# Kernel optimization log

Hardware: AMD Instinct MI355X
Metric: run time of the kernel (lower is better)

## Reference

```python
import jax, jax.numpy as jnp
import numpy as np

D, U, NNZ, B = 8192, 4096, 1_700_000, 1024

def setup_inputs() -> dict:
    key = jax.random.key(0)
    k1, k2, k3, k4 = jax.random.split(key, 4)
    x = jax.random.normal(k1, (B, D), dtype=jnp.float32)
    kernel_vector = jax.random.normal(k2, (NNZ,), dtype=jnp.float32) * 0.02
    bias = jax.random.normal(k3, (U,), dtype=jnp.float32) * 0.01
    flat = jax.random.randint(k4, (NNZ,), 0, D * U)  # random sparsity pattern
    nonzero_ind = jnp.stack([flat // U, flat % U], axis=1).astype(jnp.int32)  # [NNZ, 2]
    return {"x": x, "kernel_vector": kernel_vector, "bias": bias, "nonzero_ind": nonzero_ind}

def reference(x, kernel_vector, bias, nonzero_ind):
    # scatter_nd: build dense (D, U) kernel from nonzero entries (duplicates add, as in tf.scatter_nd)
    W = jnp.zeros((D, U), dtype=kernel_vector.dtype).at[nonzero_ind[:, 0], nonzero_ind[:, 1]].add(kernel_vector)
    out = x @ W + bias  # [B, U]
    return jnp.tanh(out)
```

## Files before the change

### kernel.cpp

```cpp
#include <hip/hip_runtime.h>
#include <hip/hip_fp16.h>
#include <cmath>

#define DIM_M 1024
#define DIM_K 8192
#define DIM_N 4096
#define SPLIT 4
#define KSPL  (DIM_K / SPLIT)
#define BKT   64
#define NT    (KSPL / BKT)
#define NB    1024
#define EPB   8192

typedef __attribute__((ext_vector_type(8))) _Float16 half8;
typedef __attribute__((ext_vector_type(4))) float floatx4;

struct __align__(8) Half4 { __half2 a, b; };

__device__ inline void gload_lds16(const void* g, void* l) {
    __builtin_amdgcn_global_load_lds(
        (const __attribute__((address_space(1))) void*)g,
        (__attribute__((address_space(3))) void*)l, 16, 0, 0);
}

__global__ void cvt_f2h(const floatx4* __restrict__ in, Half4* __restrict__ out, int n4) {
    int i = blockIdx.x * blockDim.x + threadIdx.x;
    if (i < n4) {
        floatx4 f = in[i];
        Half4 h;
        h.a = __floats2half2_rn(f.x, f.y);
        h.b = __floats2half2_rn(f.z, f.w);
        out[i] = h;
    }
}


__global__ __launch_bounds__(512) void hist_k(const int* __restrict__ ind,
                                              unsigned* __restrict__ cnt, int nnz) {
    __shared__ unsigned h[NB];
    const int tid = threadIdx.x;
    for (int i = tid; i < NB; i += 512) h[i] = 0u;
    __syncthreads();
    const int base = blockIdx.x * EPB;
    const int lim = min(nnz - base, EPB);
    const int4* ip = (const int4*)(ind + 2 * (size_t)base);
    for (int k2 = tid; k2 < lim / 2; k2 += 512) {
        int4 w = ip[k2];
        atomicAdd(&h[w.y >> 2], 1u);
        atomicAdd(&h[w.w >> 2], 1u);
    }
    if ((lim & 1) && tid == 0) {
        int u = ind[2 * (size_t)(base + lim - 1) + 1];
        atomicAdd(&h[u >> 2], 1u);
    }
    __syncthreads();
    for (int i = tid; i < NB; i += 512) cnt[(size_t)blockIdx.x * NB + i] = h[i];
}

__global__ void scanb_k(unsigned* cnt, unsigned* __restrict__ bb, int nblk) {
    __shared__ unsigned s[256];
    const int tid = threadIdx.x, bin = blockIdx.x;
    unsigned carry = 0;
    for (int c0 = 0; c0 < nblk; c0 += 256) {
        int b = c0 + tid;
        unsigned v = (b < nblk) ? cnt[(size_t)b * NB + bin] : 0u;
        s[tid] = v;
        __syncthreads();
        for (int off = 1; off < 256; off <<= 1) {
            unsigned add = (tid >= off) ? s[tid - off] : 0u;
            __syncthreads();
            s[tid] += add;
            __syncthreads();
        }
        if (b < nblk) cnt[(size_t)b * NB + bin] = carry + s[tid] - v;
        carry += s[255];
        __syncthreads();
    }
    if (tid == 0) bb[bin] = carry;
}

__global__ void scant_k(unsigned* bb) {
    __shared__ unsigned s[NB];
    const int tid = threadIdx.x;
    unsigned v = bb[tid];
    s[tid] = v;
    __syncthreads();
    for (int off = 1; off < NB; off <<= 1) {
        unsigned add = (tid >= off) ? s[tid - off] : 0u;
        __syncthreads();
        s[tid] += add;
        __syncthreads();
    }
    bb[tid] = s[tid] - v;
    if (tid == NB - 1) bb[NB] = s[tid];
}

__global__ __launch_bounds__(512) void reorder_k(const int* __restrict__ ind,
                                                 const float* __restrict__ kv,
                                                 const unsigned* __restrict__ start,
                                                 const unsigned* __restrict__ bb,
                                                 uint2* __restrict__ ebuf, int nnz) {
    extern __shared__ char rsm[];
    uint2*    buf  = (uint2*)rsm;
    unsigned* gofs = (unsigned*)(rsm + 65536);
    unsigned* cur  = (unsigned*)(rsm + 98304);
    unsigned* dl   = (unsigned*)(rsm + 102400);
    unsigned* ss   = (unsigned*)(rsm + 106496);
    const int tid = threadIdx.x, blk = blockIdx.x;
    const int base = blk * EPB;
    const int lim = min(nnz - base, EPB);
    const int4*   ip = (const int4*)(ind + 2 * (size_t)base);
    const float2* vp = (const float2*)(kv + base);

    for (int i = tid; i < NB; i += 512) cur[i] = 0u;
    __syncthreads();
    for (int k2 = tid; k2 < lim / 2; k2 += 512) {
        int4 w = ip[k2];
        atomicAdd(&cur[w.y >> 2], 1u);
        atomicAdd(&cur[w.w >> 2], 1u);
    }
    if ((lim & 1) && tid == 0) {
        int u = ind[2 * (size_t)(base + lim - 1) + 1];
        atomicAdd(&cur[u >> 2], 1u);
    }
    __syncthreads();
    unsigned c0 = cur[2 * tid], c1 = cur[2 * tid + 1];
    unsigned own = c0 + c1;
    ss[tid] = own;
    __syncthreads();
    for (int off = 1; off < 512; off <<= 1) {
        unsigned t = (tid >= off) ? ss[tid - off] : 0u;
        __syncthreads();
        ss[tid] += t;
        __syncthreads();
    }
    unsigned e0 = ss[tid] - own;
    unsigned e1 = e0 + c0;
    __syncthreads();
    cur[2 * tid]     = e0;
    cur[2 * tid + 1] = e1;
    unsigned g0 = bb[2 * tid]     + start[(size_t)blk * NB + 2 * tid];
    unsigned g1 = bb[2 * tid + 1] + start[(size_t)blk * NB + 2 * tid + 1];
    dl[2 * tid]     = g0 - e0;
    dl[2 * tid + 1] = g1 - e1;
    __syncthreads();
    for (int k2 = tid; k2 < lim / 2; k2 += 512) {
        int4 w = ip[k2];
        float2 v = vp[k2];
        int b0 = w.y >> 2, b1 = w.w >> 2;
        unsigned r0 = atomicAdd(&cur[b0], 1u);
        buf[r0]  = make_uint2(((unsigned)(w.y & 3) << 13) | (unsigned)w.x, __float_as_uint(v.x));
        gofs[r0] = dl[b0] + r0;
        unsigned r1 = atomicAdd(&cur[b1], 1u);
        buf[r1]  = make_uint2(((unsigned)(w.w & 3) << 13) | (unsigned)w.z, __float_as_uint(v.y));
        gofs[r1] = dl[b1] + r1;
    }
    if ((lim & 1) && tid == 0) {
        size_t e = (size_t)base + lim - 1;
        int d = ind[2 * e], u = ind[2 * e + 1];
        int b = u >> 2;
        unsigned r = atomicAdd(&cur[b], 1u);
        buf[r]  = make_uint2(((unsigned)(u & 3) << 13) | (unsigned)d, __float_as_uint(kv[e]));
        gofs[r] = dl[b] + r;
    }
    __syncthreads();
    for (int j = tid; j < lim; j += 512)
        ebuf[gofs[j]] = buf[j];
}

__global__ __launch_bounds__(512) void accum_k(const uint2* __restrict__ ebuf,
                                               const unsigned* __restrict__ bb,
                                               Half4* __restrict__ wh4) {
    extern __shared__ float reg[];
    floatx4* reg4 = (floatx4*)reg;
    const int tid = threadIdx.x, bin = blockIdx.x;
    for (int i = tid; i < 8192; i += 512) reg4[i] = floatx4{0.f, 0.f, 0.f, 0.f};
    __syncthreads();
    const unsigned s0 = bb[bin], s1 = bb[bin + 1];
    for (unsigned e = s0 + tid; e < s1; e += 512) {
        uint2 p = ebuf[e];
        atomicAdd(&reg[p.x], __uint_as_float(p.y));
    }
    __syncthreads();
    for (int i = tid; i < 8192; i += 512) {
        floatx4 f = reg4[i];
        Half4 h;
        h.a = __floats2half2_rn(f.x, f.y);
        h.b = __floats2half2_rn(f.z, f.w);
        wh4[(size_t)bin * 8192 + i] = h;
    }
}

__global__ __launch_bounds__(1024, 4) void gemm8_k(
    const _Float16* __restrict__ Ah,
    const _Float16* __restrict__ Bh,
    _Float16*       __restrict__ part)
{
    extern __shared__ char smem[];

    const int tid  = threadIdx.x;
    const int lane = tid & 63;
    const int wave = tid >> 6;

    const int bid = blockIdx.x;
    const int swz = (bid & 7) * 32 + (bid >> 3);
    const int n0  = (swz >> 4) * 256;
    const int rem = swz & 15;
    const int m0  = (rem >> 2) * 256;
    const int sp  = rem & 3;
    const size_t kbase = (size_t)sp * KSPL;

    const int srow = tid >> 3;
    const int sch  = (tid & 7) ^ (srow & 7);
    const _Float16* aSg = Ah + (size_t)(m0 + srow) * DIM_K + kbase + sch * 8;
    const _Float16* bSg = Bh + (size_t)(n0 + srow) * DIM_K + kbase + sch * 8;
    char* aLg = smem + wave * 1024;
    char* bLg = smem + 32768 + wave * 1024;

    const int wn  = wave & 3;
    const int wrm = wave >> 2;
    const int q   = lane >> 4;
    const int l7  = lane & 7;
    const char* aRd = smem + (wrm * 64 + (lane & 15)) * 128;
    const char* bRd = smem + 32768 + (wn * 64 + (lane & 15)) * 128;
    const int ch0 = ((0 * 4 + q) ^ l7) * 16;
    const int ch1 = ((1 * 4 + q) ^ l7) * 16;
    const int chA = (wave & 1) ? ch1 : ch0;
    const int chB = (wave & 1) ? ch0 : ch1;

    floatx4 acc[4][4] = {};
    half8 aF[4], bF[4];

#define STAGE(C)                                                              \
    { _Pragma("unroll") for (int p = 0; p < 2; ++p) {                         \
        gload_lds16(aSg + (size_t)p * (128 * DIM_K), aLg + (C) * 65536 + p * 16384); \
        gload_lds16(bSg + (size_t)p * (128 * DIM_K), bLg + (C) * 65536 + p * 16384); } \
      aSg += BKT; bSg += BKT; }

#define PH(C, CH)                                                             \
    { _Pragma("unroll") for (int i = 0; i < 4; ++i)                           \
        aF[i] = *(const half8*)(aRd + (C) * 65536 + i * 2048 + (CH));         \
      _Pragma("unroll") for (int i = 0; i < 4; ++i)                           \
        bF[i] = *(const half8*)(bRd + (C) * 65536 + i * 2048 + (CH));         \
      asm volatile("s_waitcnt lgkmcnt(0)" ::: "memory");                      \
      __builtin_amdgcn_sched_barrier(0);                                      \
      __builtin_amdgcn_s_setprio(1);                                          \
      _Pragma("unroll") for (int mi = 0; mi < 4; ++mi)                        \
        _Pragma("unroll") for (int ni = 0; ni < 4; ++ni)                      \
          acc[mi][ni] = __builtin_amdgcn_mfma_f32_16x16x32_f16(               \
              aF[mi], bF[ni], acc[mi][ni], 0, 0, 0);                          \
      __builtin_amdgcn_s_setprio(0); }

#define KTILE(C) PH(C, chA) PH(C, chB)

    STAGE(0)
    STAGE(1)
    asm volatile("s_waitcnt vmcnt(4)" ::: "memory");
    __builtin_amdgcn_s_barrier();

    for (int t2 = 0; t2 < NT / 2; ++t2) {
        KTILE(0)
        __builtin_amdgcn_s_barrier();
        if (t2 < NT / 2 - 1) {
            STAGE(0)
            asm volatile("s_waitcnt vmcnt(4)" ::: "memory");
        } else {
            asm volatile("s_waitcnt vmcnt(0)" ::: "memory");
        }
        __builtin_amdgcn_s_barrier();
        KTILE(1)
        if (t2 < NT / 2 - 1) {
            __builtin_amdgcn_s_barrier();
            STAGE(1)
            asm volatile("s_waitcnt vmcnt(4)" ::: "memory");
            __builtin_amdgcn_s_barrier();
        }
    }

#undef KTILE
#undef PH
#undef STAGE

    _Float16* pbase = part + (size_t)sp * DIM_M * DIM_N;
    #pragma unroll
    for (int ni = 0; ni < 4; ++ni) {
        const int col = n0 + wn * 64 + ni * 16 + (lane & 15);
        #pragma unroll
        for (int mi = 0; mi < 4; ++mi) {
            const int row = m0 + wrm * 64 + mi * 16 + (q << 2);
            #pragma unroll
            for (int r = 0; r < 4; ++r)
                pbase[(size_t)(row + r) * DIM_N + col] = (_Float16)acc[mi][ni][r];
        }
    }
}

__global__ void reduce_tanh(const Half4* __restrict__ part, const float* __restrict__ bias,
                            floatx4* __restrict__ out) {
    const int n4 = DIM_M * DIM_N / 4;
    int i = blockIdx.x * blockDim.x + threadIdx.x;
    if (i < n4) {
        float sx = 0.f, sy = 0.f, sz = 0.f, sw = 0.f;
        #pragma unroll
        for (int sp = 0; sp < SPLIT; ++sp) {
            Half4 p = part[(size_t)sp * n4 + i];
            float2 lo = __half22float2(p.a);
            float2 hi = __half22float2(p.b);
            sx += lo.x; sy += lo.y; sz += hi.x; sw += hi.y;
        }
        floatx4 b = ((const floatx4*)bias)[i & (DIM_N / 4 - 1)];
        floatx4 o;
        o.x = tanhf(sx + b.x);
        o.y = tanhf(sy + b.y);
        o.z = tanhf(sz + b.z);
        o.w = tanhf(sw + b.w);
        out[i] = o;
    }
}

extern "C" void kernel_launch(void* const* d_in, const int* in_sizes, int n_in,
                              void* d_out, int out_size, void* d_ws, size_t ws_size,
                              hipStream_t stream) {
    const float* x    = (const float*)d_in[0];
    const float* kv   = (const float*)d_in[1];
    const float* bias = (const float*)d_in[2];
    const int*   ind  = (const int*)d_in[3];
    float* out = (float*)d_out;
    const int nnz = in_sizes[1];

    char* ws = (char*)d_ws;
    _Float16* wh = (_Float16*)ws;
    const size_t whBytes = (size_t)DIM_N * DIM_K * 2;
    _Float16* xh = (_Float16*)(ws + whBytes);
    const size_t xhBytes = (size_t)DIM_M * DIM_K * 2;
    _Float16* part = (_Float16*)(ws + whBytes + xhBytes);
    const size_t partBytes = (size_t)SPLIT * DIM_M * DIM_N * 2;
    uint2* ebuf = (uint2*)(ws + whBytes + xhBytes + partBytes);
    const size_t ebufBytes = (size_t)16 << 20;
    unsigned* cnt = (unsigned*)(ws + whBytes + xhBytes + partBytes + ebufBytes);
    const size_t cntBytes = (size_t)1024 * NB * 4;
    unsigned* bb = (unsigned*)(ws + whBytes + xhBytes + partBytes + ebufBytes + cntBytes);

    const int xN4 = (int)((size_t)DIM_M * DIM_K / 4);
    const int oN4 = DIM_M * DIM_N / 4;
    const int nblk = (nnz + EPB - 1) / EPB;

    cvt_f2h<<<(xN4 + 255) / 256, 256, 0, stream>>>((const floatx4*)x, (Half4*)xh, xN4);
    hist_k<<<nblk, 512, 0, stream>>>(ind, cnt, nnz);
    scanb_k<<<NB, 256, 0, stream>>>(cnt, bb, nblk);
    scant_k<<<1, NB, 0, stream>>>(bb);

    hipFuncSetAttribute((const void*)reorder_k,
                        hipFuncAttributeMaxDynamicSharedMemorySize, 131072);
    reorder_k<<<nblk, 512, 110592, stream>>>(ind, kv, cnt, bb, ebuf, nnz);

    hipFuncSetAttribute((const void*)accum_k,
                        hipFuncAttributeMaxDynamicSharedMemorySize, 131072);
    accum_k<<<NB, 512, 131072, stream>>>(ebuf, bb, (Half4*)wh);

    hipFuncSetAttribute((const void*)gemm8_k,
                        hipFuncAttributeMaxDynamicSharedMemorySize, 131072);
    gemm8_k<<<dim3(256), 1024, 131072, stream>>>(xh, wh, part);

    reduce_tanh<<<(oN4 + 255) / 256, 256, 0, stream>>>((const Half4*)part, bias, (floatx4*)out);
}
```

Measured before the change: 131.8 us.

## Retile GEMM to 128x256 blocks with 32-wide K tiles and static LDS

Changes the split-K fp16 GEMM from 256x256 tiles with 1024 threads and a 64-wide K stage to 128x256 tiles with 512 threads, a 32-wide K stage and 48KB of static shared memory, launching 512 blocks instead of 256. The smaller LDS footprint and block size are meant to allow more resident blocks per CU and better spread across CUs. The cost is lower arithmetic intensity per block (A reuse halves), twice as many barriers per K step, and a new XOR swizzle for the narrower rows.

Result: slower. 136.9 us (+3.9%).

```diff
diff --git a/kernel.cpp b/kernel.cpp
--- a/kernel.cpp
+++ b/kernel.cpp
@@ -7,8 +7,8 @@
 #define DIM_N 4096
 #define SPLIT 4
 #define KSPL  (DIM_K / SPLIT)
-#define BKT   64
-#define NT    (KSPL / BKT)
+#define BKT   32
+#define NTT   (KSPL / BKT)
 #define NB    1024
 #define EPB   8192
 
@@ -191,57 +191,56 @@
     }
 }
 
-__global__ __launch_bounds__(1024, 4) void gemm8_k(
+__global__ __launch_bounds__(512, 4) void gemm8_k(
     const _Float16* __restrict__ Ah,
     const _Float16* __restrict__ Bh,
     _Float16*       __restrict__ part)
 {
-    extern __shared__ char smem[];
+    __shared__ char smem[2 * 24576];
 
     const int tid  = threadIdx.x;
     const int lane = tid & 63;
     const int wave = tid >> 6;
 
     const int bid = blockIdx.x;
-    const int swz = (bid & 7) * 32 + (bid >> 3);
-    const int n0  = (swz >> 4) * 256;
-    const int rem = swz & 15;
-    const int m0  = (rem >> 2) * 256;
-    const int sp  = rem & 3;
+    const int swz = (bid & 7) * 64 + (bid >> 3);
+    const int mt = swz & 7;
+    const int sp = (swz >> 3) & 3;
+    const int nt = swz >> 5;
+    const int m0 = mt * 128;
+    const int n0 = nt * 256;
     const size_t kbase = (size_t)sp * KSPL;
 
-    const int srow = tid >> 3;
-    const int sch  = (tid & 7) ^ (srow & 7);
+    const int srow = tid >> 2;
+    const int sch  = (tid & 3) ^ ((tid >> 3) & 3);
     const _Float16* aSg = Ah + (size_t)(m0 + srow) * DIM_K + kbase + sch * 8;
-    const _Float16* bSg = Bh + (size_t)(n0 + srow) * DIM_K + kbase + sch * 8;
-    char* aLg = smem + wave * 1024;
-    char* bLg = smem + 32768 + wave * 1024;
-
+    const _Float16* bSg0 = Bh + (size_t)(n0 + srow) * DIM_K + kbase + sch * 8;
+    const _Float16* bSg1 = Bh + (size_t)(n0 + 128 + srow) * DIM_K + kbase + sch * 8;
+    char* aL  = smem + wave * 1024;
+    char* bL0 = smem + 8192 + wave * 1024;
+    char* bL1 = smem + 16384 + wave * 1024;
+
+    const int wrm = wave >> 2;
     const int wn  = wave & 3;
-    const int wrm = wave >> 2;
     const int q   = lane >> 4;
-    const int l7  = lane & 7;
-    const char* aRd = smem + (wrm * 64 + (lane & 15)) * 128;
-    const char* bRd = smem + 32768 + (wn * 64 + (lane & 15)) * 128;
-    const int ch0 = ((0 * 4 + q) ^ l7) * 16;
-    const int ch1 = ((1 * 4 + q) ^ l7) * 16;
-    const int chA = (wave & 1) ? ch1 : ch0;
-    const int chB = (wave & 1) ? ch0 : ch1;
+    const char* aRd = smem + (wrm * 64 + (lane & 15)) * 64;
+    const char* bRd = smem + 8192 + (wn * 64 + (lane & 15)) * 64;
+    const int ch = ((lane >> 4) ^ ((lane >> 1) & 3)) * 16;
 
     floatx4 acc[4][4] = {};
     half8 aF[4], bF[4];
 
 #define STAGE(C)                                                              \
-    { _Pragma("unroll") for (int p = 0; p < 2; ++p) {                         \
-        gload_lds16(aSg + (size_t)p * (128 * DIM_K), aLg + (C) * 65536 + p * 16384); \
-        gload_lds16(bSg + (size_t)p * (128 * DIM_K), bLg + (C) * 65536 + p * 16384); } \
-      aSg += BKT; bSg += BKT; }
-
-#define PH(C, CH)                                                             \
+    { gload_lds16(aSg,  aL  + (C) * 24576);                                   \
+      gload_lds16(bSg0, bL0 + (C) * 24576);                                   \
+      gload_lds16(bSg1, bL1 + (C) * 24576);                                   \
+      aSg += BKT; bSg0 += BKT; bSg1 += BKT; }
+
+#define KTILE(C)                                                              \
     { _Pragma("unroll") for (int i = 0; i < 4; ++i)                           \
-        aF[i] = *(const half8*)(aRd + (C) * 65536 + i * 2048 + (CH));         \
+        aF[i] = *(const half8*)(aRd + (C) * 24576 + i * 1024 + ch);           \
       _Pragma("unroll") for (int i = 0; i < 4; ++i)                           \
-        bF[i] = *(const half8*)(bRd + (C) * 65536 + i * 2048 + (CH));         \
+        bF[i] = *(const half8*)(bRd + (C) * 24576 + i * 1024 + ch);           \
       asm volatile("s_waitcnt lgkmcnt(0)" ::: "memory");                      \
       __builtin_amdgcn_sched_barrier(0);                                      \
       __builtin_amdgcn_s_setprio(1);                                          \
@@ -251,34 +250,31 @@
               aF[mi], bF[ni], acc[mi][ni], 0, 0, 0);                          \
       __builtin_amdgcn_s_setprio(0); }
 
-#define KTILE(C) PH(C, chA) PH(C, chB)
-
     STAGE(0)
     STAGE(1)
-    asm volatile("s_waitcnt vmcnt(4)" ::: "memory");
+    asm volatile("s_waitcnt vmcnt(3)" ::: "memory");
     __builtin_amdgcn_s_barrier();
 
-    for (int t2 = 0; t2 < NT / 2; ++t2) {
+    for (int t2 = 0; t2 < NTT / 2; ++t2) {
         KTILE(0)
         __builtin_amdgcn_s_barrier();
-        if (t2 < NT / 2 - 1) {
+        if (t2 < NTT / 2 - 1) {
             STAGE(0)
-            asm volatile("s_waitcnt vmcnt(4)" ::: "memory");
+            asm volatile("s_waitcnt vmcnt(3)" ::: "memory");
         } else {
             asm volatile("s_waitcnt vmcnt(0)" ::: "memory");
         }
         __builtin_amdgcn_s_barrier();
         KTILE(1)
-        if (t2 < NT / 2 - 1) {
+        if (t2 < NTT / 2 - 1) {
             __builtin_amdgcn_s_barrier();
             STAGE(1)
-            asm volatile("s_waitcnt vmcnt(4)" ::: "memory");
+            asm volatile("s_waitcnt vmcnt(3)" ::: "memory");
             __builtin_amdgcn_s_barrier();
         }
     }
 
 #undef KTILE
-#undef PH
 #undef STAGE
 
     _Float16* pbase = part + (size_t)sp * DIM_M * DIM_N;
@@ -358,9 +354,7 @@
                         hipFuncAttributeMaxDynamicSharedMemorySize, 131072);
     accum_k<<<NB, 512, 131072, stream>>>(ebuf, bb, (Half4*)wh);
 
-    hipFuncSetAttribute((const void*)gemm8_k,
-                        hipFuncAttributeMaxDynamicSharedMemorySize, 131072);
-    gemm8_k<<<dim3(256), 1024, 131072, stream>>>(xh, wh, part);
+    gemm8_k<<<dim3(512), 512, 0, stream>>>(xh, wh, part);
 
     reduce_tanh<<<(oN4 + 255) / 256, 256, 0, stream>>>((const Half4*)part, bias, (floatx4*)out);
 }
```

## Restructure GEMM to 8 waves with 4-stage K32 LDS pipeline

Applied to the files above, without the earlier changes.

The fp16 GEMM kernel now runs 512 threads per block instead of 1024, with each wave computing a 128x64 tile (8x4 MFMA accumulators) rather than 64x64. The K tile shrinks from 64 to 32 and the LDS ring grows from 2 to 4 buffers, with A and B loads issued inside the two compute phases of each K tile. The intent is to raise per-wave data reuse and hide global-to-LDS latency with a deeper prefetch. In exchange each thread holds twice the accumulator registers, blocks synchronise more often, and the swizzle pattern changes.

Result: slower. 135.9 us (+3.1%).

```diff
diff --git a/kernel.cpp b/kernel.cpp
--- a/kernel.cpp
+++ b/kernel.cpp
@@ -7,8 +7,8 @@
 #define DIM_N 4096
 #define SPLIT 4
 #define KSPL  (DIM_K / SPLIT)
-#define BKT   64
-#define NT    (KSPL / BKT)
+#define BKT   32
+#define NTT   (KSPL / BKT)
 #define NB    1024
 #define EPB   8192
 
@@ -191,7 +191,7 @@
     }
 }
 
-__global__ __launch_bounds__(1024, 4) void gemm8_k(
+__global__ __launch_bounds__(512, 2) void gemm8_k(
     const _Float16* __restrict__ Ah,
     const _Float16* __restrict__ Bh,
     _Float16*       __restrict__ part)
@@ -210,38 +210,37 @@
     const int sp  = rem & 3;
     const size_t kbase = (size_t)sp * KSPL;
 
-    const int srow = tid >> 3;
-    const int sch  = (tid & 7) ^ (srow & 7);
+    const int srow = tid >> 2;
+    const int sch  = (tid & 3) ^ ((tid >> 3) & 3);
     const _Float16* aSg = Ah + (size_t)(m0 + srow) * DIM_K + kbase + sch * 8;
     const _Float16* bSg = Bh + (size_t)(n0 + srow) * DIM_K + kbase + sch * 8;
-    char* aLg = smem + wave * 1024;
-    char* bLg = smem + 32768 + wave * 1024;
-
+    const int wofs = wave * 1024;
+
+    const int wrm = wave >> 2;
     const int wn  = wave & 3;
-    const int wrm = wave >> 2;
     const int q   = lane >> 4;
-    const int l7  = lane & 7;
-    const char* aRd = smem + (wrm * 64 + (lane & 15)) * 128;
-    const char* bRd = smem + 32768 + (wn * 64 + (lane & 15)) * 128;
-    const int ch0 = ((0 * 4 + q) ^ l7) * 16;
-    const int ch1 = ((1 * 4 + q) ^ l7) * 16;
-    const int chA = (wave & 1) ? ch1 : ch0;
-    const int chB = (wave & 1) ? ch0 : ch1;
-
-    floatx4 acc[4][4] = {};
+    const char* aRd = smem + (wrm * 128 + (lane & 15)) * 64;
+    const char* bRd = smem + 16384 + (wn * 64 + (lane & 15)) * 64;
+    const int ch = (q ^ ((lane >> 1) & 3)) * 16;
+
+    floatx4 acc[8][4] = {};
     half8 aF[4], bF[4];
 
-#define STAGE(C)                                                              \
-    { _Pragma("unroll") for (int p = 0; p < 2; ++p) {                         \
-        gload_lds16(aSg + (size_t)p * (128 * DIM_K), aLg + (C) * 65536 + p * 16384); \
-        gload_lds16(bSg + (size_t)p * (128 * DIM_K), bLg + (C) * 65536 + p * 16384); } \
-      aSg += BKT; bSg += BKT; }
-
-#define PH(C, CH)                                                             \
+#define STA(SB)                                                               \
+    { gload_lds16(aSg,                         smem + (SB) * 32768 + wofs);   \
+      gload_lds16(aSg + (size_t)128 * DIM_K,   smem + (SB) * 32768 + 8192 + wofs); }
+#define STB(SB)                                                               \
+    { gload_lds16(bSg,                         smem + (SB) * 32768 + 16384 + wofs); \
+      gload_lds16(bSg + (size_t)128 * DIM_K,   smem + (SB) * 32768 + 24576 + wofs); }
+#define ADV() { aSg += BKT; bSg += BKT; }
+
+#define PH0(CB, SB)                                                           \
     { _Pragma("unroll") for (int i = 0; i < 4; ++i)                           \
-        aF[i] = *(const half8*)(aRd + (C) * 65536 + i * 2048 + (CH));         \
+        aF[i] = *(const half8*)(aRd + (CB) * 32768 + i * 1024 + ch);          \
       _Pragma("unroll") for (int i = 0; i < 4; ++i)                           \
-        bF[i] = *(const half8*)(bRd + (C) * 65536 + i * 2048 + (CH));         \
+        bF[i] = *(const half8*)(bRd + (CB) * 32768 + i * 1024 + ch);          \
+      STA(SB)                                                                 \
+      __builtin_amdgcn_s_barrier();                                           \
       asm volatile("s_waitcnt lgkmcnt(0)" ::: "memory");                      \
       __builtin_amdgcn_sched_barrier(0);                                      \
       __builtin_amdgcn_s_setprio(1);                                          \
@@ -249,45 +248,54 @@
         _Pragma("unroll") for (int ni = 0; ni < 4; ++ni)                      \
           acc[mi][ni] = __builtin_amdgcn_mfma_f32_16x16x32_f16(               \
               aF[mi], bF[ni], acc[mi][ni], 0, 0, 0);                          \
-      __builtin_amdgcn_s_setprio(0); }
-
-#define KTILE(C) PH(C, chA) PH(C, chB)
-
-    STAGE(0)
-    STAGE(1)
-    asm volatile("s_waitcnt vmcnt(4)" ::: "memory");
+      __builtin_amdgcn_s_setprio(0);                                          \
+      __builtin_amdgcn_s_barrier(); }
+
+#define PH1(CB, SB)                                                           \
+    { _Pragma("unroll") for (int i = 0; i < 4; ++i)                           \
+        aF[i] = *(const half8*)(aRd + (CB) * 32768 + 4096 + i * 1024 + ch);   \
+      STB(SB) ADV()                                                           \
+      __builtin_amdgcn_s_barrier();                                           \
+      asm volatile("s_waitcnt lgkmcnt(0)" ::: "memory");                      \
+      __builtin_amdgcn_sched_barrier(0);                                      \
+      __builtin_amdgcn_s_setprio(1);                                          \
+      _Pragma("unroll") for (int mi = 0; mi < 4; ++mi)                        \
+        _Pragma("unroll") for (int ni = 0; ni < 4; ++ni)                      \
+          acc[4 + mi][ni] = __builtin_amdgcn_mfma_f32_16x16x32_f16(           \
+              aF[mi], bF[ni], acc[4 + mi][ni], 0, 0, 0);                      \
+      __builtin_amdgcn_s_setprio(0);                                          \
+      asm volatile("s_waitcnt vmcnt(8)" ::: "memory");                        \
+      __builtin_amdgcn_s_barrier(); }
+
+#define KTILE(CB, SB) PH0(CB, SB) PH1(CB, SB)
+
+    STA(0) STB(0) ADV()
+    STA(1) STB(1) ADV()
+    STA(2) STB(2) ADV()
+    asm volatile("s_waitcnt vmcnt(8)" ::: "memory");
     __builtin_amdgcn_s_barrier();
 
-    for (int t2 = 0; t2 < NT / 2; ++t2) {
-        KTILE(0)
-        __builtin_amdgcn_s_barrier();
-        if (t2 < NT / 2 - 1) {
-            STAGE(0)
-            asm volatile("s_waitcnt vmcnt(4)" ::: "memory");
-        } else {
-            asm volatile("s_waitcnt vmcnt(0)" ::: "memory");
-        }
-        __builtin_amdgcn_s_barrier();
-        KTILE(1)
-        if (t2 < NT / 2 - 1) {
-            __builtin_amdgcn_s_barrier();
-            STAGE(1)
-            asm volatile("s_waitcnt vmcnt(4)" ::: "memory");
-            __builtin_amdgcn_s_barrier();
-        }
+    for (int it = 0; it < NTT / 4; ++it) {
+        KTILE(0, 3)
+        KTILE(1, 0)
+        KTILE(2, 1)
+        KTILE(3, 2)
     }
 
 #undef KTILE
-#undef PH
-#undef STAGE
+#undef PH1
+#undef PH0
+#undef ADV
+#undef STB
+#undef STA
 
     _Float16* pbase = part + (size_t)sp * DIM_M * DIM_N;
     #pragma unroll
     for (int ni = 0; ni < 4; ++ni) {
         const int col = n0 + wn * 64 + ni * 16 + (lane & 15);
         #pragma unroll
-        for (int mi = 0; mi < 4; ++mi) {
-            const int row = m0 + wrm * 64 + mi * 16 + (q << 2);
+        for (int mi = 0; mi < 8; ++mi) {
+            const int row = m0 + wrm * 128 + mi * 16 + (q << 2);
             #pragma unroll
             for (int r = 0; r < 4; ++r)
                 pbase[(size_t)(row + r) * DIM_N + col] = (_Float16)acc[mi][ni][r];
@@ -360,7 +368,7 @@
 
     hipFuncSetAttribute((const void*)gemm8_k,
                         hipFuncAttributeMaxDynamicSharedMemorySize, 131072);
-    gemm8_k<<<dim3(256), 1024, 131072, stream>>>(xh, wh, part);
+    gemm8_k<<<dim3(256), 512, 131072, stream>>>(xh, wh, part);
 
     reduce_tanh<<<(oN4 + 255) / 256, 256, 0, stream>>>((const Half4*)part, bias, (floatx4*)out);
 }
```

## Replace global bucket sort with per-block local clustering and segment offsets

Applied to the files above, without the earlier changes.

Drops the histogram and two scan kernels and turns the reorder kernel into a per-block local clustering that writes its bin offsets table and block-sorted entries straight to ebuf. The accumulate kernel now walks every source block's segment for its bin instead of one contiguous range. This removes three launches and the global scatter, at the cost of roughly 208 short, uneven segment loops per accumulate block spread over only 208 of its 512 threads. It also drops the per-wave alternation of ch0/ch1 order in the GEMM's LDS reads.

Measured after the change: 125.2 us. 5.0% less time.

```diff
diff --git a/kernel.cpp b/kernel.cpp
--- a/kernel.cpp
+++ b/kernel.cpp
@@ -34,78 +34,15 @@
     }
 }
 
-
-__global__ __launch_bounds__(512) void hist_k(const int* __restrict__ ind,
-                                              unsigned* __restrict__ cnt, int nnz) {
-    __shared__ unsigned h[NB];
-    const int tid = threadIdx.x;
-    for (int i = tid; i < NB; i += 512) h[i] = 0u;
-    __syncthreads();
-    const int base = blockIdx.x * EPB;
-    const int lim = min(nnz - base, EPB);
-    const int4* ip = (const int4*)(ind + 2 * (size_t)base);
-    for (int k2 = tid; k2 < lim / 2; k2 += 512) {
-        int4 w = ip[k2];
-        atomicAdd(&h[w.y >> 2], 1u);
-        atomicAdd(&h[w.w >> 2], 1u);
-    }
-    if ((lim & 1) && tid == 0) {
-        int u = ind[2 * (size_t)(base + lim - 1) + 1];
-        atomicAdd(&h[u >> 2], 1u);
-    }
-    __syncthreads();
-    for (int i = tid; i < NB; i += 512) cnt[(size_t)blockIdx.x * NB + i] = h[i];
-}
-
-__global__ void scanb_k(unsigned* cnt, unsigned* __restrict__ bb, int nblk) {
-    __shared__ unsigned s[256];
-    const int tid = threadIdx.x, bin = blockIdx.x;
-    unsigned carry = 0;
-    for (int c0 = 0; c0 < nblk; c0 += 256) {
-        int b = c0 + tid;
-        unsigned v = (b < nblk) ? cnt[(size_t)b * NB + bin] : 0u;
-        s[tid] = v;
-        __syncthreads();
-        for (int off = 1; off < 256; off <<= 1) {
-            unsigned add = (tid >= off) ? s[tid - off] : 0u;
-            __syncthreads();
-            s[tid] += add;
-            __syncthreads();
-        }
-        if (b < nblk) cnt[(size_t)b * NB + bin] = carry + s[tid] - v;
-        carry += s[255];
-        __syncthreads();
-    }
-    if (tid == 0) bb[bin] = carry;
-}
-
-__global__ void scant_k(unsigned* bb) {
-    __shared__ unsigned s[NB];
-    const int tid = threadIdx.x;
-    unsigned v = bb[tid];
-    s[tid] = v;
-    __syncthreads();
-    for (int off = 1; off < NB; off <<= 1) {
-        unsigned add = (tid >= off) ? s[tid - off] : 0u;
-        __syncthreads();
-        s[tid] += add;
-        __syncthreads();
-    }
-    bb[tid] = s[tid] - v;
-    if (tid == NB - 1) bb[NB] = s[tid];
-}
-
-__global__ __launch_bounds__(512) void reorder_k(const int* __restrict__ ind,
+__global__ __launch_bounds__(512) void cluster_k(const int* __restrict__ ind,
                                                  const float* __restrict__ kv,
-                                                 const unsigned* __restrict__ start,
-                                                 const unsigned* __restrict__ bb,
-                                                 uint2* __restrict__ ebuf, int nnz) {
-    extern __shared__ char rsm[];
-    uint2*    buf  = (uint2*)rsm;
-    unsigned* gofs = (unsigned*)(rsm + 65536);
-    unsigned* cur  = (unsigned*)(rsm + 98304);
-    unsigned* dl   = (unsigned*)(rsm + 102400);
-    unsigned* ss   = (unsigned*)(rsm + 106496);
+                                                 uint2* __restrict__ ebuf,
+                                                 unsigned* __restrict__ ofs,
+                                                 int nnz) {
+    extern __shared__ char csm[];
+    uint2*    buf = (uint2*)csm;
+    unsigned* cur = (unsigned*)(csm + 65536);
+    unsigned* ss  = (unsigned*)(csm + 69632);
     const int tid = threadIdx.x, blk = blockIdx.x;
     const int base = blk * EPB;
     const int lim = min(nnz - base, EPB);
@@ -139,47 +76,47 @@
     __syncthreads();
     cur[2 * tid]     = e0;
     cur[2 * tid + 1] = e1;
-    unsigned g0 = bb[2 * tid]     + start[(size_t)blk * NB + 2 * tid];
-    unsigned g1 = bb[2 * tid + 1] + start[(size_t)blk * NB + 2 * tid + 1];
-    dl[2 * tid]     = g0 - e0;
-    dl[2 * tid + 1] = g1 - e1;
+    unsigned* obase = ofs + (size_t)blk * (NB + 1);
+    obase[2 * tid]     = e0;
+    obase[2 * tid + 1] = e1;
+    if (tid == 511) obase[NB] = ss[511];
     __syncthreads();
     for (int k2 = tid; k2 < lim / 2; k2 += 512) {
         int4 w = ip[k2];
         float2 v = vp[k2];
-        int b0 = w.y >> 2, b1 = w.w >> 2;
-        unsigned r0 = atomicAdd(&cur[b0], 1u);
-        buf[r0]  = make_uint2(((unsigned)(w.y & 3) << 13) | (unsigned)w.x, __float_as_uint(v.x));
-        gofs[r0] = dl[b0] + r0;
-        unsigned r1 = atomicAdd(&cur[b1], 1u);
-        buf[r1]  = make_uint2(((unsigned)(w.w & 3) << 13) | (unsigned)w.z, __float_as_uint(v.y));
-        gofs[r1] = dl[b1] + r1;
+        unsigned r0 = atomicAdd(&cur[w.y >> 2], 1u);
+        buf[r0] = make_uint2(((unsigned)(w.y & 3) << 13) | (unsigned)w.x, __float_as_uint(v.x));
+        unsigned r1 = atomicAdd(&cur[w.w >> 2], 1u);
+        buf[r1] = make_uint2(((unsigned)(w.w & 3) << 13) | (unsigned)w.z, __float_as_uint(v.y));
     }
     if ((lim & 1) && tid == 0) {
         size_t e = (size_t)base + lim - 1;
         int d = ind[2 * e], u = ind[2 * e + 1];
-        int b = u >> 2;
-        unsigned r = atomicAdd(&cur[b], 1u);
-        buf[r]  = make_uint2(((unsigned)(u & 3) << 13) | (unsigned)d, __float_as_uint(kv[e]));
-        gofs[r] = dl[b] + r;
+        unsigned r = atomicAdd(&cur[u >> 2], 1u);
+        buf[r] = make_uint2(((unsigned)(u & 3) << 13) | (unsigned)d, __float_as_uint(kv[e]));
     }
     __syncthreads();
     for (int j = tid; j < lim; j += 512)
-        ebuf[gofs[j]] = buf[j];
+        ebuf[(size_t)blk * EPB + j] = buf[j];
 }
 
 __global__ __launch_bounds__(512) void accum_k(const uint2* __restrict__ ebuf,
-                                               const unsigned* __restrict__ bb,
+                                               const unsigned* __restrict__ ofs,
+                                               int nblk,
                                                Half4* __restrict__ wh4) {
     extern __shared__ float reg[];
     floatx4* reg4 = (floatx4*)reg;
     const int tid = threadIdx.x, bin = blockIdx.x;
     for (int i = tid; i < 8192; i += 512) reg4[i] = floatx4{0.f, 0.f, 0.f, 0.f};
     __syncthreads();
-    const unsigned s0 = bb[bin], s1 = bb[bin + 1];
-    for (unsigned e = s0 + tid; e < s1; e += 512) {
-        uint2 p = ebuf[e];
-        atomicAdd(&reg[p.x], __uint_as_float(p.y));
+    for (int sb = tid; sb < nblk; sb += 512) {
+        const unsigned* ob = ofs + (size_t)sb * (NB + 1) + bin;
+        unsigned o0 = ob[0], o1 = ob[1];
+        const uint2* p = ebuf + (size_t)sb * EPB;
+        for (unsigned e = o0; e < o1; ++e) {
+            uint2 v = p[e];
+            atomicAdd(&reg[v.x], __uint_as_float(v.y));
+        }
     }
     __syncthreads();
     for (int i = tid; i < 8192; i += 512) {
@@ -225,8 +162,6 @@
     const char* bRd = smem + 32768 + (wn * 64 + (lane & 15)) * 128;
     const int ch0 = ((0 * 4 + q) ^ l7) * 16;
     const int ch1 = ((1 * 4 + q) ^ l7) * 16;
-    const int chA = (wave & 1) ? ch1 : ch0;
-    const int chB = (wave & 1) ? ch0 : ch1;
 
     floatx4 acc[4][4] = {};
     half8 aF[4], bF[4];
@@ -251,7 +186,7 @@
               aF[mi], bF[ni], acc[mi][ni], 0, 0, 0);                          \
       __builtin_amdgcn_s_setprio(0); }
 
-#define KTILE(C) PH(C, chA) PH(C, chB)
+#define KTILE(C) PH(C, ch0) PH(C, ch1)
 
     STAGE(0)
     STAGE(1)
@@ -337,26 +272,21 @@
     const size_t partBytes = (size_t)SPLIT * DIM_M * DIM_N * 2;
     uint2* ebuf = (uint2*)(ws + whBytes + xhBytes + partBytes);
     const size_t ebufBytes = (size_t)16 << 20;
-    unsigned* cnt = (unsigned*)(ws + whBytes + xhBytes + partBytes + ebufBytes);
-    const size_t cntBytes = (size_t)1024 * NB * 4;
-    unsigned* bb = (unsigned*)(ws + whBytes + xhBytes + partBytes + ebufBytes + cntBytes);
+    unsigned* ofs = (unsigned*)(ws + whBytes + xhBytes + partBytes + ebufBytes);
 
     const int xN4 = (int)((size_t)DIM_M * DIM_K / 4);
     const int oN4 = DIM_M * DIM_N / 4;
     const int nblk = (nnz + EPB - 1) / EPB;
 
     cvt_f2h<<<(xN4 + 255) / 256, 256, 0, stream>>>((const floatx4*)x, (Half4*)xh, xN4);
-    hist_k<<<nblk, 512, 0, stream>>>(ind, cnt, nnz);
-    scanb_k<<<NB, 256, 0, stream>>>(cnt, bb, nblk);
-    scant_k<<<1, NB, 0, stream>>>(bb);
-
-    hipFuncSetAttribute((const void*)reorder_k,
-                        hipFuncAttributeMaxDynamicSharedMemorySize, 131072);
-    reorder_k<<<nblk, 512, 110592, stream>>>(ind, kv, cnt, bb, ebuf, nnz);
+
+    hipFuncSetAttribute((const void*)cluster_k,
+                        hipFuncAttributeMaxDynamicSharedMemorySize, 71680);
+    cluster_k<<<nblk, 512, 71680, stream>>>(ind, kv, ebuf, ofs, nnz);
 
     hipFuncSetAttribute((const void*)accum_k,
                         hipFuncAttributeMaxDynamicSharedMemorySize, 131072);
-    accum_k<<<NB, 512, 131072, stream>>>(ebuf, bb, (Half4*)wh);
+    accum_k<<<NB, 512, 131072, stream>>>(ebuf, ofs, nblk, (Half4*)wh);
 
     hipFuncSetAttribute((const void*)gemm8_k,
                         hipFuncAttributeMaxDynamicSharedMemorySize, 131072);
```
